# Optimization experiments

Measured on AMD Instinct MI355X. Metric: run time of the kernel, lower is better.

The kernel has to match this reference:

```python
import jax, jax.numpy as jnp
import numpy as np

SUB1 = 0.5
SUB2 = 0.2

def setup_inputs() -> dict:
    key = jax.random.key(0)
    kx, kw, kb = jax.random.split(key, 3)
    x = jax.random.normal(kx, (32, 16, 256, 256), dtype=jnp.float32)
    # Conv2d weight [C_out, C_in, K, K], PyTorch default init scale ~ 1/sqrt(fan_in)
    fan_in = 16 * 3 * 3
    bound = 1.0 / np.sqrt(fan_in)
    conv_weight = jax.random.uniform(kw, (16, 16, 3, 3), dtype=jnp.float32, minval=-bound, maxval=bound)
    conv_bias = jax.random.uniform(kb, (16,), dtype=jnp.float32, minval=-bound, maxval=bound)
    return {"x": x, "conv_weight": conv_weight, "conv_bias": conv_bias}

def mish(v):
    # mish(v) = v * tanh(softplus(v))
    return v * jnp.tanh(jax.nn.softplus(v))

def reference(x, conv_weight, conv_bias):
    # valid conv, stride 1, NCHW / OIHW
    y = jax.lax.conv_general_dilated(
        x, conv_weight,
        window_strides=(1, 1),
        padding='VALID',
        dimension_numbers=('NCHW', 'OIHW', 'NCHW'))
    y = y + conv_bias[None, :, None, None]
    y = y - (SUB1 + SUB2)
    return mish(y)
```

## Files before the change

kernel.cpp:

```cpp
#include <hip/hip_runtime.h>
#include <hip/hip_bf16.h>

constexpr int N   = 32;
constexpr int C   = 16;
constexpr int H   = 256;
constexpr int W   = 256;
constexpr int CO  = 16;
constexpr int OH  = 254;
constexpr int OW  = 254;
constexpr float SUBV = 0.7f;

constexpr int KPAD = 160;

constexpr int TY     = 10;
constexpr int TIN_Y  = TY + 2;
constexpr int TX     = 64;
constexpr int TIN_XS = 68;
constexpr int SITE_US = 8;
constexpr int ROW_US  = TIN_XS * SITE_US;
constexpr int PS      = TIN_Y * ROW_US;

using short8  = __attribute__((ext_vector_type(8))) short;
using floatx4 = __attribute__((ext_vector_type(4))) float;

__device__ inline uint bf16u(float f) {
    uint u = __builtin_bit_cast(uint, f);
    u += 0x7fffu + ((u >> 16) & 1u);
    return u >> 16;
}
__device__ inline uint pkbf(float lo, float hi) {
    __hip_bfloat162 h = __float22bfloat162_rn(make_float2(lo, hi));
    uint r;
    __builtin_memcpy(&r, &h, sizeof(r));
    return r;
}

__global__ void reorder_weights(const float* __restrict__ w,
                                const float* __restrict__ b,
                                ushort* __restrict__ wr) {
    const int t = threadIdx.x;
    for (int i = t; i < CO * KPAD; i += 256) {
        const int co = i / KPAD;
        const int k  = i - co * KPAD;
        ushort v = 0;
        if (k < 144) {
            const int pair = k >> 4;
            const int ci   = k & 15;
            const int ky   = pair / 3;
            const int kx   = pair - 3 * ky;
            v = (ushort)bf16u(w[((co * C + ci) * 3 + ky) * 3 + kx]);
        }
        wr[i] = v;
    }
    if (t < CO) ((float*)(wr + CO * KPAD))[t] = b[t] - SUBV;
}

__launch_bounds__(256, 4)
__global__ void conv_mfma(const float* __restrict__ x,
                          const ushort* __restrict__ wr,
                          float* __restrict__ out) {
    __shared__ ushort lds[2 * PS];

    const int tid  = threadIdx.x;
    const int lane = tid & 63;
    const int wave = tid >> 6;
    const int quad = lane >> 4;
    const int n    = lane & 15;

    const int x0 = blockIdx.x * TX;
    const int y0 = blockIdx.y * TY;
    const int ni = blockIdx.z;

    const bool active = tid < TIN_Y * (TIN_XS / 4);
    int yy = 0, qx = 0;
    float4 v[16];
    if (active) {
        yy = tid / 17;
        qx = tid - yy * 17;
        const int iy = (y0 + yy < H - 1) ? (y0 + yy) : (H - 1);
        int bx = x0 + qx * 4;
        if (bx > W - 4) bx = W - 4;
        const float* src = x + (size_t)ni * C * H * W + (size_t)iy * W + bx;
        #pragma unroll
        for (int ci = 0; ci < C; ++ci)
            v[ci] = *(const float4*)(src + (size_t)ci * H * W);
    }

    short8 afrag[5];
    {
        const ushort* wbase = wr + n * KPAD + quad * 8;
        #pragma unroll
        for (int c = 0; c < 5; ++c)
            afrag[c] = *(const short8*)(wbase + c * 32);
    }
    float bias_j[4];
    {
        const float* bp = (const float*)(wr + CO * KPAD);
        const float4 bv = *(const float4*)(bp + quad * 4);
        bias_j[0] = bv.x; bias_j[1] = bv.y; bias_j[2] = bv.z; bias_j[3] = bv.w;
    }
    int boff[5];
    #pragma unroll
    for (int c = 0; c < 5; ++c) {
        int pair = 2 * c + (quad >> 1);
        if (pair > 8) pair = 8;
        const int ky = pair / 3;
        const int kx = pair - 3 * ky;
        boff[c] = (quad & 1) * PS + ky * ROW_US + (n + kx) * SITE_US;
    }
    size_t obase[4];
    const int oxv = x0 + wave * 16 + n;
    const bool oxok = oxv < OW;
    #pragma unroll
    for (int j = 0; j < 4; ++j)
        obase[j] = ((size_t)(ni * CO + quad * 4 + j)) * OH * OW + oxv;

    if (active) {
        ushort* d = &lds[(yy * TIN_XS + qx * 4) * SITE_US];
        #pragma unroll
        for (int j = 0; j < 4; ++j) {
            ushort* d0 = d + j * SITE_US;
            *(uint4*)d0 = make_uint4(pkbf(v[0][j],  v[1][j]),  pkbf(v[2][j],  v[3][j]),
                                     pkbf(v[4][j],  v[5][j]),  pkbf(v[6][j],  v[7][j]));
            *(uint4*)(d0 + PS) = make_uint4(pkbf(v[8][j],  v[9][j]),  pkbf(v[10][j], v[11][j]),
                                            pkbf(v[12][j], v[13][j]), pkbf(v[14][j], v[15][j]));
        }
    }
    __syncthreads();

    const ushort* wcol = lds + wave * 16 * SITE_US;
    #pragma unroll 1
    for (int r = 0; r < TY; r += 2) {
        floatx4 acc0 = {0.f, 0.f, 0.f, 0.f};
        floatx4 acc1 = {0.f, 0.f, 0.f, 0.f};
        const ushort* b0 = wcol + r * ROW_US;
        const ushort* b1 = b0 + ROW_US;
        #pragma unroll
        for (int c = 0; c < 5; ++c) {
            const short8 f0 = *(const short8*)(b0 + boff[c]);
            const short8 f1 = *(const short8*)(b1 + boff[c]);
            acc0 = __builtin_amdgcn_mfma_f32_16x16x32_bf16(afrag[c], f0, acc0, 0, 0, 0);
            acc1 = __builtin_amdgcn_mfma_f32_16x16x32_bf16(afrag[c], f1, acc1, 0, 0, 0);
        }
        #pragma unroll
        for (int rr = 0; rr < 2; ++rr) {
            const int oy = y0 + r + rr;
            if (oy < OH && oxok) {
                const floatx4 av = rr ? acc1 : acc0;
                #pragma unroll
                for (int j = 0; j < 4; ++j) {
                    const float v2 = av[j] + bias_j[j];
                    const float vc = fminf(v2, 15.0f);
                    const float e  = __expf(vc);
                    const float z  = 1.0f + e;
                    const float z2 = z * z;
                    const float t  = __fdividef(z2 - 1.0f, z2 + 1.0f);
                    out[obase[j] + (size_t)oy * OW] = v2 * t;
                }
            }
        }
    }
}

extern "C" void kernel_launch(void* const* d_in, const int* in_sizes, int n_in,
                              void* d_out, int out_size, void* d_ws, size_t ws_size,
                              hipStream_t stream) {
    const float* x = (const float*)d_in[0];
    const float* w = (const float*)d_in[1];
    const float* b = (const float*)d_in[2];
    float* out = (float*)d_out;
    ushort* wr = (ushort*)d_ws;

    hipLaunchKernelGGL(reorder_weights, dim3(1), dim3(256), 0, stream, w, b, wr);

    dim3 grid(OW / TX + 1, (OH + TY - 1) / TY, N);
    hipLaunchKernelGGL(conv_mfma, grid, dim3(256), 0, stream, x, wr, out);
}
```

Measured before the change: 288.3 us.

## Pre-convert input to channels-last bf16 and stage tiles via direct global-to-LDS loads

```diff
diff --git a/kernel.cpp b/kernel.cpp
--- a/kernel.cpp
+++ b/kernel.cpp
@@ -16,9 +16,12 @@
 constexpr int TIN_Y  = TY + 2;
 constexpr int TX     = 64;
 constexpr int TIN_XS = 68;
-constexpr int SITE_US = 8;
+constexpr int SITE_US = 16;
 constexpr int ROW_US  = TIN_XS * SITE_US;
-constexpr int PS      = TIN_Y * ROW_US;
+constexpr int NCHUNK  = 26;
+constexpr int LDS_US  = NCHUNK * 512;
+
+constexpr size_t XB_BYTES = (size_t)N * H * W * C * 2;
 
 using short8  = __attribute__((ext_vector_type(8))) short;
 using floatx4 = __attribute__((ext_vector_type(4))) float;
@@ -33,6 +36,11 @@
     uint r;
     __builtin_memcpy(&r, &h, sizeof(r));
     return r;
+}
+__device__ inline void load_lds16(const void* g, void* l) {
+    __builtin_amdgcn_global_load_lds(
+        (const __attribute__((address_space(1))) void*)g,
+        (__attribute__((address_space(3))) void*)l, 16, 0, 0);
 }
 
 __global__ void reorder_weights(const float* __restrict__ w,
@@ -55,11 +63,36 @@
     if (t < CO) ((float*)(wr + CO * KPAD))[t] = b[t] - SUBV;
 }
 
-__launch_bounds__(256, 4)
-__global__ void conv_mfma(const float* __restrict__ x,
-                          const ushort* __restrict__ wr,
-                          float* __restrict__ out) {
-    __shared__ ushort lds[2 * PS];
+__launch_bounds__(256)
+__global__ void convert_x(const float* __restrict__ x, ushort* __restrict__ xb) {
+    const size_t t = (size_t)blockIdx.x * 256 + threadIdx.x;
+    const int ni = (int)(t >> 15);
+    const int sp = (int)(t & 32767);
+    const int y  = sp >> 7;
+    const int xp = (sp & 127) << 1;
+    const float* src = x + ((size_t)ni * C * H) * W + (size_t)y * W + xp;
+    float px[16], py[16];
+    #pragma unroll
+    for (int ci = 0; ci < C; ++ci) {
+        const float2 p = *(const float2*)(src + (size_t)ci * H * W);
+        px[ci] = p.x; py[ci] = p.y;
+    }
+    uint4* dst = (uint4*)(xb + t * 32);
+    dst[0] = make_uint4(pkbf(px[0],px[1]),  pkbf(px[2],px[3]),
+                        pkbf(px[4],px[5]),  pkbf(px[6],px[7]));
+    dst[1] = make_uint4(pkbf(px[8],px[9]),  pkbf(px[10],px[11]),
+                        pkbf(px[12],px[13]),pkbf(px[14],px[15]));
+    dst[2] = make_uint4(pkbf(py[0],py[1]),  pkbf(py[2],py[3]),
+                        pkbf(py[4],py[5]),  pkbf(py[6],py[7]));
+    dst[3] = make_uint4(pkbf(py[8],py[9]),  pkbf(py[10],py[11]),
+                        pkbf(py[12],py[13]),pkbf(py[14],py[15]));
+}
+
+__launch_bounds__(256, 6)
+__global__ void conv_mfma2(const ushort* __restrict__ xb,
+                           const ushort* __restrict__ wr,
+                           float* __restrict__ out) {
+    __shared__ ushort lds[LDS_US];
 
     const int tid  = threadIdx.x;
     const int lane = tid & 63;
@@ -71,19 +104,15 @@
     const int y0 = blockIdx.y * TY;
     const int ni = blockIdx.z;
 
-    const bool active = tid < TIN_Y * (TIN_XS / 4);
-    int yy = 0, qx = 0;
-    float4 v[16];
-    if (active) {
-        yy = tid / 17;
-        qx = tid - yy * 17;
-        const int iy = (y0 + yy < H - 1) ? (y0 + yy) : (H - 1);
-        int bx = x0 + qx * 4;
-        if (bx > W - 4) bx = W - 4;
-        const float* src = x + (size_t)ni * C * H * W + (size_t)iy * W + bx;
-        #pragma unroll
-        for (int ci = 0; ci < C; ++ci)
-            v[ci] = *(const float4*)(src + (size_t)ci * H * W);
+    for (int c = wave; c < NCHUNK; c += 4) {
+        const int S  = c * 32 + (lane >> 1);
+        const int h  = lane & 1;
+        const int yy = S / TIN_XS;
+        const int xx = S - TIN_XS * yy;
+        const int iy = min(y0 + yy, H - 1);
+        const int ix = min(x0 + xx, W - 1);
+        const ushort* src = xb + (((size_t)ni * H + iy) * W + ix) * 16 + h * 8;
+        load_lds16(src, (char*)lds + c * 1024);
     }
 
     short8 afrag[5];
@@ -106,7 +135,7 @@
         if (pair > 8) pair = 8;
         const int ky = pair / 3;
         const int kx = pair - 3 * ky;
-        boff[c] = (quad & 1) * PS + ky * ROW_US + (n + kx) * SITE_US;
+        boff[c] = ky * ROW_US + (n + kx) * SITE_US + (quad & 1) * 8;
     }
     size_t obase[4];
     const int oxv = x0 + wave * 16 + n;
@@ -115,17 +144,6 @@
     for (int j = 0; j < 4; ++j)
         obase[j] = ((size_t)(ni * CO + quad * 4 + j)) * OH * OW + oxv;
 
-    if (active) {
-        ushort* d = &lds[(yy * TIN_XS + qx * 4) * SITE_US];
-        #pragma unroll
-        for (int j = 0; j < 4; ++j) {
-            ushort* d0 = d + j * SITE_US;
-            *(uint4*)d0 = make_uint4(pkbf(v[0][j],  v[1][j]),  pkbf(v[2][j],  v[3][j]),
-                                     pkbf(v[4][j],  v[5][j]),  pkbf(v[6][j],  v[7][j]));
-            *(uint4*)(d0 + PS) = make_uint4(pkbf(v[8][j],  v[9][j]),  pkbf(v[10][j], v[11][j]),
-                                            pkbf(v[12][j], v[13][j]), pkbf(v[14][j], v[15][j]));
-        }
-    }
     __syncthreads();
 
     const ushort* wcol = lds + wave * 16 * SITE_US;
@@ -162,6 +180,113 @@
     }
 }
 
+__launch_bounds__(256, 4)
+__global__ void conv_mfma_fb(const float* __restrict__ x,
+                             const ushort* __restrict__ wr,
+                             float* __restrict__ out) {
+    __shared__ ushort lds[2 * 6528];
+
+    const int tid  = threadIdx.x;
+    const int lane = tid & 63;
+    const int wave = tid >> 6;
+    const int quad = lane >> 4;
+    const int n    = lane & 15;
+
+    const int x0 = blockIdx.x * TX;
+    const int y0 = blockIdx.y * TY;
+    const int ni = blockIdx.z;
+
+    const bool active = tid < TIN_Y * (TIN_XS / 4);
+    int yy = 0, qx = 0;
+    float4 v[16];
+    if (active) {
+        yy = tid / 17;
+        qx = tid - yy * 17;
+        const int iy = (y0 + yy < H - 1) ? (y0 + yy) : (H - 1);
+        int bx = x0 + qx * 4;
+        if (bx > W - 4) bx = W - 4;
+        const float* src = x + (size_t)ni * C * H * W + (size_t)iy * W + bx;
+        #pragma unroll
+        for (int ci = 0; ci < C; ++ci)
+            v[ci] = *(const float4*)(src + (size_t)ci * H * W);
+    }
+
+    short8 afrag[5];
+    {
+        const ushort* wbase = wr + n * KPAD + quad * 8;
+        #pragma unroll
+        for (int c = 0; c < 5; ++c)
+            afrag[c] = *(const short8*)(wbase + c * 32);
+    }
+    float bias_j[4];
+    {
+        const float* bp = (const float*)(wr + CO * KPAD);
+        const float4 bv = *(const float4*)(bp + quad * 4);
+        bias_j[0] = bv.x; bias_j[1] = bv.y; bias_j[2] = bv.z; bias_j[3] = bv.w;
+    }
+    int boff[5];
+    #pragma unroll
+    for (int c = 0; c < 5; ++c) {
+        int pair = 2 * c + (quad >> 1);
+        if (pair > 8) pair = 8;
+        const int ky = pair / 3;
+        const int kx = pair - 3 * ky;
+        boff[c] = (quad & 1) * 6528 + ky * 544 + (n + kx) * 8;
+    }
+    size_t obase[4];
+    const int oxv = x0 + wave * 16 + n;
+    const bool oxok = oxv < OW;
+    #pragma unroll
+    for (int j = 0; j < 4; ++j)
+        obase[j] = ((size_t)(ni * CO + quad * 4 + j)) * OH * OW + oxv;
+
+    if (active) {
+        ushort* d = &lds[(yy * TIN_XS + qx * 4) * 8];
+        #pragma unroll
+        for (int j = 0; j < 4; ++j) {
+            ushort* d0 = d + j * 8;
+            *(uint4*)d0 = make_uint4(pkbf(v[0][j],  v[1][j]),  pkbf(v[2][j],  v[3][j]),
+                                     pkbf(v[4][j],  v[5][j]),  pkbf(v[6][j],  v[7][j]));
+            *(uint4*)(d0 + 6528) = make_uint4(pkbf(v[8][j],  v[9][j]),  pkbf(v[10][j], v[11][j]),
+                                              pkbf(v[12][j], v[13][j]), pkbf(v[14][j], v[15][j]));
+        }
+    }
+    __syncthreads();
+
+    const ushort* wcol = lds + wave * 16 * 8;
+    #pragma unroll 1
+    for (int r = 0; r < TY; r += 2) {
+        floatx4 acc0 = {0.f, 0.f, 0.f, 0.f};
+        floatx4 acc1 = {0.f, 0.f, 0.f, 0.f};
+        const ushort* b0 = wcol + r * 544;
+        const ushort* b1 = b0 + 544;
+        #pragma unroll
+        for (int c = 0; c < 5; ++c) {
+            const short8 f0 = *(const short8*)(b0 + boff[c]);
+            const short8 f1 = *(const short8*)(b1 + boff[c]);
+            acc0 = __builtin_amdgcn_mfma_f32_16x16x32_bf16(afrag[c], f0, acc0, 0, 0, 0);
+            acc1 = __builtin_amdgcn_mfma_f32_16x16x32_bf16(afrag[c], f1, acc1, 0, 0, 0);
+        }
+        #pragma unroll
+        for (int rr = 0; rr < 2; ++rr) {
+            const int oy = y0 + r + rr;
+            if (oy < OH && oxok) {
+                const floatx4 av = rr ? acc1 : acc0;
+                #pragma unroll
+                for (int j = 0; j < 4; ++j) {
+                    const float v2 = av[j] + bias_j[j];
+                    const float vc = fminf(v2, 15.0f);
+                    const float e  = __expf(vc);
+                    const float z  = 1.0f + e;
+                    const float z2 = z * z;
+                    const float t  = __fdividef(z2 - 1.0f, z2 + 1.0f);
+                    out[obase[j] + (size_t)oy * OW] = v2 * t;
+                }
+            }
+        }
+    }
+}
+
 extern "C" void kernel_launch(void* const* d_in, const int* in_sizes, int n_in,
                               void* d_out, int out_size, void* d_ws, size_t ws_size,
                               hipStream_t stream) {
@@ -169,10 +294,19 @@
     const float* w = (const float*)d_in[1];
     const float* b = (const float*)d_in[2];
     float* out = (float*)d_out;
-    ushort* wr = (ushort*)d_ws;
-
-    hipLaunchKernelGGL(reorder_weights, dim3(1), dim3(256), 0, stream, w, b, wr);
-
-    dim3 grid(OW / TX + 1, (OH + TY - 1) / TY, N);
-    hipLaunchKernelGGL(conv_mfma, grid, dim3(256), 0, stream, x, wr, out);
-}
+
+    const size_t need = XB_BYTES + 5184;
+    if (ws_size >= need) {
+        ushort* xb = (ushort*)d_ws;
+        ushort* wr = (ushort*)((char*)d_ws + XB_BYTES);
+        hipLaunchKernelGGL(reorder_weights, dim3(1), dim3(256), 0, stream, w, b, wr);
+        hipLaunchKernelGGL(convert_x, dim3((N * H * W / 2) / 256), dim3(256), 0, stream, x, xb);
+        dim3 grid(OW / TX + 1, (OH + TY - 1) / TY, N);
+        hipLaunchKernelGGL(conv_mfma2, grid, dim3(256), 0, stream, xb, wr, out);
+    } else {
+        ushort* wr = (ushort*)d_ws;
+        hipLaunchKernelGGL(reorder_weights, dim3(1), dim3(256), 0, stream, w, b, wr);
+        dim3 grid(OW / TX + 1, (OH + TY - 1) / TY, N);
+        hipLaunchKernelGGL(conv_mfma_fb, grid, dim3(256), 0, stream, x, wr, out);
+    }
+}
```

After: 286.5 us. About the same (-0.6%).

## Stage input tile via global_load_lds then convert to interleaved bf16 in LDS

Applied to the files above, without the earlier changes.

```diff
diff --git a/kernel.cpp b/kernel.cpp
--- a/kernel.cpp
+++ b/kernel.cpp
@@ -12,13 +12,17 @@
 
 constexpr int KPAD = 160;
 
-constexpr int TY     = 10;
+constexpr int TY     = 6;
 constexpr int TIN_Y  = TY + 2;
 constexpr int TX     = 64;
 constexpr int TIN_XS = 68;
-constexpr int SITE_US = 8;
+constexpr int SITE_US = 16;
 constexpr int ROW_US  = TIN_XS * SITE_US;
-constexpr int PS      = TIN_Y * ROW_US;
+constexpr int BF_US   = TIN_Y * ROW_US;
+constexpr int FROW_CH   = 17;
+constexpr int FPLANE_CH = TIN_Y * FROW_CH;
+constexpr int F_CH      = C * FPLANE_CH;
+constexpr int FPL_F     = FPLANE_CH * 4;
 
 using short8  = __attribute__((ext_vector_type(8))) short;
 using floatx4 = __attribute__((ext_vector_type(4))) float;
@@ -33,6 +37,11 @@
     uint r;
     __builtin_memcpy(&r, &h, sizeof(r));
     return r;
+}
+__device__ inline void load_lds16(const void* g, void* l) {
+    __builtin_amdgcn_global_load_lds(
+        (const __attribute__((address_space(1))) void*)g,
+        (__attribute__((address_space(3))) void*)l, 16, 0, 0);
 }
 
 __global__ void reorder_weights(const float* __restrict__ w,
@@ -55,11 +64,12 @@
     if (t < CO) ((float*)(wr + CO * KPAD))[t] = b[t] - SUBV;
 }
 
-__launch_bounds__(256, 4)
-__global__ void conv_mfma(const float* __restrict__ x,
-                          const ushort* __restrict__ wr,
-                          float* __restrict__ out) {
-    __shared__ ushort lds[2 * PS];
+__launch_bounds__(256, 3)
+__global__ void conv_fused(const float* __restrict__ x,
+                           const ushort* __restrict__ wr,
+                           float* __restrict__ out) {
+    __shared__ float  lds_f[F_CH * 4];
+    __shared__ ushort lds_bf[BF_US];
 
     const int tid  = threadIdx.x;
     const int lane = tid & 63;
@@ -71,19 +81,19 @@
     const int y0 = blockIdx.y * TY;
     const int ni = blockIdx.z;
 
-    const bool active = tid < TIN_Y * (TIN_XS / 4);
-    int yy = 0, qx = 0;
-    float4 v[16];
-    if (active) {
-        yy = tid / 17;
-        qx = tid - yy * 17;
-        const int iy = (y0 + yy < H - 1) ? (y0 + yy) : (H - 1);
-        int bx = x0 + qx * 4;
-        if (bx > W - 4) bx = W - 4;
-        const float* src = x + (size_t)ni * C * H * W + (size_t)iy * W + bx;
-        #pragma unroll
-        for (int ci = 0; ci < C; ++ci)
-            v[ci] = *(const float4*)(src + (size_t)ci * H * W);
+    {
+        const float* xs = x + (size_t)ni * C * H * W;
+        for (int c = wave; c < F_CH / 64; c += 4) {
+            const int L   = c * 64 + lane;
+            const int ci  = L / FPLANE_CH;
+            const int rem = L - ci * FPLANE_CH;
+            const int yy  = rem / FROW_CH;
+            const int q   = rem - yy * FROW_CH;
+            const int iy  = min(y0 + yy, H - 1);
+            const int ix  = min(x0 + 4 * q, W - 4);
+            const float* src = xs + ((size_t)ci * H + iy) * W + ix;
+            load_lds16(src, (char*)lds_f + c * 1024);
+        }
     }
 
     short8 afrag[5];
@@ -106,7 +116,7 @@
         if (pair > 8) pair = 8;
         const int ky = pair / 3;
         const int kx = pair - 3 * ky;
-        boff[c] = (quad & 1) * PS + ky * ROW_US + (n + kx) * SITE_US;
+        boff[c] = ky * ROW_US + (n + kx) * SITE_US + (quad & 1) * 8;
     }
     size_t obase[4];
     const int oxv = x0 + wave * 16 + n;
@@ -115,20 +125,25 @@
     for (int j = 0; j < 4; ++j)
         obase[j] = ((size_t)(ni * CO + quad * 4 + j)) * OH * OW + oxv;
 
-    if (active) {
-        ushort* d = &lds[(yy * TIN_XS + qx * 4) * SITE_US];
+    __syncthreads();
+
+    for (int it = tid; it < TIN_Y * TIN_XS * 2; it += 256) {
+        const int s  = it >> 1;
+        const int h  = it & 1;
+        const int yy = s / TIN_XS;
+        const int xx = s - yy * TIN_XS;
+        const float* fp = lds_f + (8 * h) * FPL_F + yy * (FROW_CH * 4) + xx;
+        float f[8];
         #pragma unroll
-        for (int j = 0; j < 4; ++j) {
-            ushort* d0 = d + j * SITE_US;
-            *(uint4*)d0 = make_uint4(pkbf(v[0][j],  v[1][j]),  pkbf(v[2][j],  v[3][j]),
-                                     pkbf(v[4][j],  v[5][j]),  pkbf(v[6][j],  v[7][j]));
-            *(uint4*)(d0 + PS) = make_uint4(pkbf(v[8][j],  v[9][j]),  pkbf(v[10][j], v[11][j]),
-                                            pkbf(v[12][j], v[13][j]), pkbf(v[14][j], v[15][j]));
-        }
+        for (int j = 0; j < 8; ++j)
+            f[j] = fp[j * FPL_F];
+        *(uint4*)(lds_bf + (size_t)it * 8) =
+            make_uint4(pkbf(f[0], f[1]), pkbf(f[2], f[3]),
+                       pkbf(f[4], f[5]), pkbf(f[6], f[7]));
     }
     __syncthreads();
 
-    const ushort* wcol = lds + wave * 16 * SITE_US;
+    const ushort* wcol = lds_bf + wave * 16 * SITE_US;
     #pragma unroll 1
     for (int r = 0; r < TY; r += 2) {
         floatx4 acc0 = {0.f, 0.f, 0.f, 0.f};
@@ -174,5 +189,5 @@
     hipLaunchKernelGGL(reorder_weights, dim3(1), dim3(256), 0, stream, w, b, wr);
 
     dim3 grid(OW / TX + 1, (OH + TY - 1) / TY, N);
-    hipLaunchKernelGGL(conv_mfma, grid, dim3(256), 0, stream, x, wr, out);
+    hipLaunchKernelGGL(conv_fused, grid, dim3(256), 0, stream, x, wr, out);
 }
```

Result: no change. 283.2 us (-1.8%).
